# Kernel optimization log

Measured on AMD Instinct MI355X. Metric: run time of the kernel, lower is better.

The kernel has to match this reference:

```python
import jax, jax.numpy as jnp
import numpy as np

TAU = 2.0  # LIF membrane time constant (tau=2.0)
V_TH = 1.0  # spiking threshold (spikingjelly default)

@jax.custom_vjp
def spike(v):
    # Heaviside spike at v >= 0 (input is v - V_TH)
    return (v >= 0.0).astype(v.dtype)

def _spike_fwd(v):
    return spike(v), v

def _spike_bwd(v, g):
    # ATan surrogate gradient (spikingjelly default, alpha=2):
    # d/dv = alpha / (2 * (1 + (pi/2 * alpha * v)^2)) = 1 / (1 + (pi*v)^2)
    return (g / (1.0 + (jnp.pi * v) ** 2),)

spike.defvjp(_spike_fwd, _spike_bwd)

def lif_linear(x, w):
    """SpikLinearLayer: Linear (no bias) then multi-step LIF over leading T axis.
    x: [T, B, N, Din], w: [Dout, Din] -> spikes [T, B, N, Dout]
    LIF: v <- v + (y - v)/tau ; s = H(v - vth) ; hard reset v <- v*(1-s)
    """
    y = jnp.einsum('tbnd,ed->tbne', x, w)
    def step(v, yt):
        v = v + (yt - v) / TAU
        s = spike(v - V_TH)
        return v * (1.0 - s), s
    _, spikes = jax.lax.scan(step, jnp.zeros_like(y[0]), y)
    return spikes

def setup_inputs() -> dict:
    key = jax.random.key(0)
    k0, k1, k2, k3 = jax.random.split(key, 4)
    T, B, N, D, L = 4, 32, 1024, 256, 2
    x = jax.random.normal(k0, (T, B, N, D), dtype=jnp.float32)
    w_in = jax.random.normal(k1, (2 * D, D), dtype=jnp.float32) * 0.05
    w_hidden = jax.random.normal(k2, (L, 2 * D, 2 * D), dtype=jnp.float32) * 0.05
    w_out = jax.random.normal(k3, (D, 2 * D), dtype=jnp.float32) * 0.05
    return {"x": x, "w_in": w_in, "w_hidden": w_hidden, "w_out": w_out}

def reference(x, w_in, w_hidden, w_out):
    # TemporalBlock.forward
    h = lif_linear(x, w_in)                       # [T,B,N,2D]
    for l in range(w_hidden.shape[0]):
        h = h * (1.0 - lif_linear(h, w_hidden[l]))  # multiplicative spike gate
    return lif_linear(h, w_out)                   # [T,B,N,D]
```

## Files before the change

### kernel.cpp

```cpp
#include <hip/hip_runtime.h>
#include <stdint.h>

typedef __attribute__((ext_vector_type(8))) short short8;
typedef __attribute__((ext_vector_type(4))) float f32x4;

constexpr int T_ = 4;
constexpr int BNTOT = 32768;

__device__ __forceinline__ void gload_lds16(const void* g, void* lds) {
    __builtin_amdgcn_global_load_lds(
        (const __attribute__((address_space(1))) void*)g,
        (__attribute__((address_space(3))) void*)lds, 16, 0, 0);
}

__device__ __forceinline__ uint32_t bf1(float f) {
    uint32_t x = __builtin_bit_cast(uint32_t, f);
    return (x + 0x7FFFu + ((x >> 16) & 1u)) >> 16;
}
__device__ __forceinline__ uint32_t pk(float lo, float hi) {
    return bf1(lo) | (bf1(hi) << 16);
}

__global__ __launch_bounds__(256)
void cvt_bf16(const float* __restrict__ in, ushort* __restrict__ out) {
    const size_t i = ((size_t)blockIdx.x * 256 + threadIdx.x) * 8;
    const float4 a = *(const float4*)(in + i);
    const float4 b = *(const float4*)(in + i + 4);
    uint4 o;
    o.x = pk(a.x, a.y); o.y = pk(a.z, a.w);
    o.z = pk(b.x, b.y); o.w = pk(b.z, b.w);
    *(uint4*)(out + i) = o;
}

template <int MODE, int K, int NOUT>
__global__ __launch_bounds__(256, 2)
void lif_mfma(const ushort* __restrict__ A,
              const float* __restrict__ W,
              void* __restrict__ Out)
{
    __shared__ __align__(16) char smem[81920];

    constexpr int NS = K / 64;
    constexpr int NCOLT = NOUT / 64;

    const int tid = threadIdx.x;
    const int l   = tid & 63;
    const int w   = tid >> 6;

    const int id  = blockIdx.x;
    const int xcd = id & 7;
    const int j_  = id >> 3;
    const int row0 = (xcd * 64 + j_ / NCOLT) * 64;
    const int col0 = (j_ % NCOLT) * 64;

    const int rowbyte = (l & 15) << 7;
    const int gx = l >> 4;
    const int sw = l & 7;

    f32x4 acc[4][4];
#pragma unroll
    for (int m = 0; m < 4; ++m)
#pragma unroll
        for (int n = 0; n < 4; ++n) acc[m][n] = (f32x4)0.f;

    const int a_rowin = l >> 3;
    const int a_gsrc  = (l & 7) ^ a_rowin;
    const ushort* a_base = A + (size_t)(w * BNTOT + row0 + a_rowin) * K + a_gsrc * 8;

    const int bc  = tid >> 2;
    const int bkq = tid & 3;
    const float* w_base = W + (size_t)(col0 + bc) * K + bkq * 16;
    const int b_g0 = (bkq * 2)     ^ (bc & 7);
    const int b_g1 = (bkq * 2 + 1) ^ (bc & 7);

    auto stageA = [&](int s, int buf) {
        const ushort* ap = a_base + (size_t)s * 64;
        char* ad = smem + buf * 32768 + w * 8192;
#pragma unroll
        for (int i = 0; i < 8; ++i)
            gload_lds16(ap + (size_t)i * 8 * K, ad + i * 1024);
    };
    auto writeB = [&](const float4& b0, const float4& b1,
                      const float4& b2, const float4& b3, int buf) {
        char* bd = smem + 65536 + buf * 8192 + bc * 128;
        uint4 lo, hi;
        lo.x = pk(b0.x, b0.y); lo.y = pk(b0.z, b0.w);
        lo.z = pk(b1.x, b1.y); lo.w = pk(b1.z, b1.w);
        hi.x = pk(b2.x, b2.y); hi.y = pk(b2.z, b2.w);
        hi.z = pk(b3.x, b3.y); hi.w = pk(b3.z, b3.w);
        *(uint4*)(bd + b_g0 * 16) = lo;
        *(uint4*)(bd + b_g1 * 16) = hi;
    };

    {
        const float* wp = w_base;
        float4 b0 = *(const float4*)(wp);
        float4 b1 = *(const float4*)(wp + 4);
        float4 b2 = *(const float4*)(wp + 8);
        float4 b3 = *(const float4*)(wp + 12);
        stageA(0, 0);
        writeB(b0, b1, b2, b3, 0);
    }
    __syncthreads();

    int buf = 0;
    for (int s = 0; s < NS; ++s) {
        const bool more = (s + 1 < NS);
        float4 b0, b1, b2, b3;
        if (more) {
            const float* wp = w_base + (s + 1) * 64;
            b0 = *(const float4*)(wp);
            b1 = *(const float4*)(wp + 4);
            b2 = *(const float4*)(wp + 8);
            b3 = *(const float4*)(wp + 12);
            stageA(s + 1, buf ^ 1);
        }
        {
            const char* at = smem + buf * 32768 + w * 8192;
            const char* bt = smem + 65536 + buf * 8192;
#pragma unroll
            for (int kk = 0; kk < 2; ++kk) {
                const int go = (((kk * 4 + gx) ^ sw) << 4);
                short8 af[4], bfr[4];
#pragma unroll
                for (int m = 0; m < 4; ++m)
                    af[m] = *(const short8*)(at + m * 2048 + rowbyte + go);
#pragma unroll
                for (int n = 0; n < 4; ++n)
                    bfr[n] = *(const short8*)(bt + n * 2048 + rowbyte + go);
#pragma unroll
                for (int m = 0; m < 4; ++m)
#pragma unroll
                    for (int n = 0; n < 4; ++n)
                        acc[m][n] = __builtin_amdgcn_mfma_f32_16x16x32_bf16(
                            af[m], bfr[n], acc[m][n], 0, 0, 0);
            }
        }
        if (more) writeB(b0, b1, b2, b3, buf ^ 1);
        __syncthreads();
        buf ^= 1;
    }

    {
        float* Yw = (float*)smem + w * 4096;
#pragma unroll
        for (int m = 0; m < 4; ++m)
#pragma unroll
            for (int n = 0; n < 4; ++n)
#pragma unroll
                for (int j = 0; j < 4; ++j) {
                    const int row = m * 16 + gx * 4 + j;
                    const int colp = (n * 16 + (l & 15)) ^ (((row >> 2) & 1) << 4);
                    Yw[row * 64 + colp] = acc[m][n][j];
                }
    }
    __syncthreads();
    {
        const int rr0 = tid >> 5;
        const int c2  = (tid & 31) * 2;
#pragma unroll
        for (int rb = 0; rb < 8; ++rb) {
            const int row = rb * 8 + rr0;
            const int cp  = c2 ^ (((row >> 2) & 1) << 4);
            float v0 = 0.f, v1 = 0.f;
#pragma unroll
            for (int t = 0; t < T_; ++t) {
                const float* Yt = (const float*)smem + t * 4096 + row * 64;
                const float y0 = Yt[cp], y1 = Yt[cp + 1];
                v0 = 0.5f * (v0 + y0);
                v1 = 0.5f * (v1 + y1);
                const bool s0 = (v0 >= 1.f), s1 = (v1 >= 1.f);
                v0 = s0 ? 0.f : v0;
                v1 = s1 ? 0.f : v1;
                const size_t orow = (size_t)(t * BNTOT + row0 + row);
                if (MODE == 0) {
                    uint32_t u = (s0 ? 0x3F80u : 0u) | (s1 ? 0x3F800000u : 0u);
                    *(uint32_t*)((ushort*)Out + orow * NOUT + col0 + c2) = u;
                } else if (MODE == 1) {
                    const uint32_t h = *(const uint32_t*)(A + orow * K + col0 + c2);
                    const uint32_t msk = (s0 ? 0u : 0xFFFFu) | (s1 ? 0u : 0xFFFF0000u);
                    *(uint32_t*)((ushort*)Out + orow * NOUT + col0 + c2) = h & msk;
                } else {
                    float2 o;
                    o.x = s0 ? 1.f : 0.f;
                    o.y = s1 ? 1.f : 0.f;
                    *(float2*)((float*)Out + orow * NOUT + col0 + c2) = o;
                }
            }
        }
    }
}

extern "C" void kernel_launch(void* const* d_in, const int* in_sizes, int n_in,
                              void* d_out, int out_size, void* d_ws, size_t ws_size,
                              hipStream_t stream)
{
    const float* x     = (const float*)d_in[0];
    const float* w_in  = (const float*)d_in[1];
    const float* w_h   = (const float*)d_in[2];
    const float* w_out = (const float*)d_in[3];

    ushort* xbf = (ushort*)d_out;
    ushort* hA  = (ushort*)d_ws;
    ushort* hB  = (ushort*)d_out;
    float*  out = (float*)d_out;

    cvt_bf16<<<16384, 256, 0, stream>>>(x, xbf);

    lif_mfma<0, 256, 512><<<8 * 512, 256, 0, stream>>>(xbf, w_in, hA);
    lif_mfma<1, 512, 512><<<8 * 512, 256, 0, stream>>>(hA, w_h, hB);
    lif_mfma<1, 512, 512><<<8 * 512, 256, 0, stream>>>(hB, w_h + 512 * 512, hA);
    lif_mfma<2, 512, 256><<<4 * 512, 256, 0, stream>>>(hA, w_out, out);
}
```

Before: 421.2 us.

## Halve K-tile and LDS footprint to raise occupancy to four blocks per CU

The K step shrinks from 64 to 32, which halves the A/B LDS staging buffers, with new swizzles for the narrower rows. The epilogue now writes the accumulator tile in two 32-column halves so the 40KB buffer can hold it, and launch bounds rise to four blocks per CU. The aim is more resident waves to hide global-load latency. The cost is twice as many loop iterations and barriers, less MFMA work per sync, and extra barriers in the epilogue.

```diff
diff --git a/kernel.cpp b/kernel.cpp
--- a/kernel.cpp
+++ b/kernel.cpp
@@ -33,14 +33,14 @@
 }
 
 template <int MODE, int K, int NOUT>
-__global__ __launch_bounds__(256, 2)
+__global__ __launch_bounds__(256, 4)
 void lif_mfma(const ushort* __restrict__ A,
               const float* __restrict__ W,
               void* __restrict__ Out)
 {
-    __shared__ __align__(16) char smem[81920];
+    __shared__ __align__(16) char smem[40960];
 
-    constexpr int NS = K / 64;
+    constexpr int NS = K / 32;
     constexpr int NCOLT = NOUT / 64;
 
     const int tid = threadIdx.x;
@@ -53,9 +53,8 @@
     const int row0 = (xcd * 64 + j_ / NCOLT) * 64;
     const int col0 = (j_ % NCOLT) * 64;
 
-    const int rowbyte = (l & 15) << 7;
-    const int gx = l >> 4;
-    const int sw = l & 7;
+    const int rby = (l & 15) * 64;
+    const int gp  = ((l >> 4) ^ ((l >> 1) & 3)) << 4;
 
     f32x4 acc[4][4];
 #pragma unroll
@@ -63,131 +62,117 @@
 #pragma unroll
         for (int n = 0; n < 4; ++n) acc[m][n] = (f32x4)0.f;
 
-    const int a_rowin = l >> 3;
-    const int a_gsrc  = (l & 7) ^ a_rowin;
-    const ushort* a_base = A + (size_t)(w * BNTOT + row0 + a_rowin) * K + a_gsrc * 8;
+    const int a_gsrc = (l & 3) ^ ((l >> 3) & 3);
+    const ushort* a_base = A + ((size_t)(w * BNTOT + row0) + (l >> 2)) * K + a_gsrc * 8;
 
-    const int bc  = tid >> 2;
-    const int bkq = tid & 3;
-    const float* w_base = W + (size_t)(col0 + bc) * K + bkq * 16;
-    const int b_g0 = (bkq * 2)     ^ (bc & 7);
-    const int b_g1 = (bkq * 2 + 1) ^ (bc & 7);
+    const int b_col  = tid >> 2;
+    const int b_gsrc = (tid & 3) ^ ((tid >> 3) & 3);
+    const float* w_base = W + (size_t)(col0 + b_col) * K + b_gsrc * 8;
 
     auto stageA = [&](int s, int buf) {
-        const ushort* ap = a_base + (size_t)s * 64;
-        char* ad = smem + buf * 32768 + w * 8192;
+        const ushort* ap = a_base + s * 32;
+        char* ad = smem + buf * 16384 + w * 4096;
 #pragma unroll
-        for (int i = 0; i < 8; ++i)
-            gload_lds16(ap + (size_t)i * 8 * K, ad + i * 1024);
+        for (int j = 0; j < 4; ++j)
+            gload_lds16(ap + (size_t)j * 16 * K, ad + j * 1024);
     };
-    auto writeB = [&](const float4& b0, const float4& b1,
-                      const float4& b2, const float4& b3, int buf) {
-        char* bd = smem + 65536 + buf * 8192 + bc * 128;
-        uint4 lo, hi;
-        lo.x = pk(b0.x, b0.y); lo.y = pk(b0.z, b0.w);
-        lo.z = pk(b1.x, b1.y); lo.w = pk(b1.z, b1.w);
-        hi.x = pk(b2.x, b2.y); hi.y = pk(b2.z, b2.w);
-        hi.z = pk(b3.x, b3.y); hi.w = pk(b3.z, b3.w);
-        *(uint4*)(bd + b_g0 * 16) = lo;
-        *(uint4*)(bd + b_g1 * 16) = hi;
+    auto writeB = [&](const float4& f0, const float4& f1, int buf) {
+        uint4 o;
+        o.x = pk(f0.x, f0.y); o.y = pk(f0.z, f0.w);
+        o.z = pk(f1.x, f1.y); o.w = pk(f1.z, f1.w);
+        *(uint4*)(smem + 32768 + buf * 4096 + b_col * 64 + (tid & 3) * 16) = o;
     };
 
     {
-        const float* wp = w_base;
-        float4 b0 = *(const float4*)(wp);
-        float4 b1 = *(const float4*)(wp + 4);
-        float4 b2 = *(const float4*)(wp + 8);
-        float4 b3 = *(const float4*)(wp + 12);
+        const float4 f0 = *(const float4*)(w_base);
+        const float4 f1 = *(const float4*)(w_base + 4);
         stageA(0, 0);
-        writeB(b0, b1, b2, b3, 0);
+        writeB(f0, f1, 0);
     }
     __syncthreads();
 
     int buf = 0;
     for (int s = 0; s < NS; ++s) {
         const bool more = (s + 1 < NS);
-        float4 b0, b1, b2, b3;
+        float4 f0, f1;
         if (more) {
-            const float* wp = w_base + (s + 1) * 64;
-            b0 = *(const float4*)(wp);
-            b1 = *(const float4*)(wp + 4);
-            b2 = *(const float4*)(wp + 8);
-            b3 = *(const float4*)(wp + 12);
+            const float* wp = w_base + (s + 1) * 32;
+            f0 = *(const float4*)(wp);
+            f1 = *(const float4*)(wp + 4);
             stageA(s + 1, buf ^ 1);
         }
         {
-            const char* at = smem + buf * 32768 + w * 8192;
-            const char* bt = smem + 65536 + buf * 8192;
+            const char* at = smem + buf * 16384 + w * 4096;
+            const char* bt = smem + 32768 + buf * 4096;
+            short8 af[4], bfr[4];
 #pragma unroll
-            for (int kk = 0; kk < 2; ++kk) {
-                const int go = (((kk * 4 + gx) ^ sw) << 4);
-                short8 af[4], bfr[4];
+            for (int m = 0; m < 4; ++m)
+                af[m] = *(const short8*)(at + m * 1024 + rby + gp);
 #pragma unroll
-                for (int m = 0; m < 4; ++m)
-                    af[m] = *(const short8*)(at + m * 2048 + rowbyte + go);
+            for (int n = 0; n < 4; ++n)
+                bfr[n] = *(const short8*)(bt + n * 1024 + rby + gp);
+#pragma unroll
+            for (int m = 0; m < 4; ++m)
 #pragma unroll
                 for (int n = 0; n < 4; ++n)
-                    bfr[n] = *(const short8*)(bt + n * 2048 + rowbyte + go);
-#pragma unroll
-                for (int m = 0; m < 4; ++m)
-#pragma unroll
-                    for (int n = 0; n < 4; ++n)
-                        acc[m][n] = __builtin_amdgcn_mfma_f32_16x16x32_bf16(
-                            af[m], bfr[n], acc[m][n], 0, 0, 0);
-            }
+                    acc[m][n] = __builtin_amdgcn_mfma_f32_16x16x32_bf16(
+                        af[m], bfr[n], acc[m][n], 0, 0, 0);
         }
-        if (more) writeB(b0, b1, b2, b3, buf ^ 1);
+        if (more) writeB(f0, f1, buf ^ 1);
         __syncthreads();
         buf ^= 1;
     }
 
-    {
-        float* Yw = (float*)smem + w * 4096;
+    float* Y = (float*)smem;
 #pragma unroll
-        for (int m = 0; m < 4; ++m)
+    for (int half = 0; half < 2; ++half) {
 #pragma unroll
-            for (int n = 0; n < 4; ++n)
+        for (int nn = 0; nn < 2; ++nn) {
+            const int n = half * 2 + nn;
+#pragma unroll
+            for (int m = 0; m < 4; ++m)
 #pragma unroll
                 for (int j = 0; j < 4; ++j) {
-                    const int row = m * 16 + gx * 4 + j;
-                    const int colp = (n * 16 + (l & 15)) ^ (((row >> 2) & 1) << 4);
-                    Yw[row * 64 + colp] = acc[m][n][j];
+                    const int row = m * 16 + (l >> 4) * 4 + j;
+                    const int cl  = nn * 16 + (l & 15);
+                    const int colp = cl ^ (((row >> 2) & 1) << 4);
+                    Y[w * 2048 + row * 32 + colp] = acc[m][n][j];
                 }
-    }
-    __syncthreads();
-    {
-        const int rr0 = tid >> 5;
-        const int c2  = (tid & 31) * 2;
+        }
+        __syncthreads();
 #pragma unroll
-        for (int rb = 0; rb < 8; ++rb) {
-            const int row = rb * 8 + rr0;
-            const int cp  = c2 ^ (((row >> 2) & 1) << 4);
+        for (int u4 = 0; u4 < 4; ++u4) {
+            const int u   = u4 * 256 + tid;
+            const int row = u >> 4;
+            const int cp  = (u & 15) * 2;
+            const int colp = cp ^ (((row >> 2) & 1) << 4);
             float v0 = 0.f, v1 = 0.f;
 #pragma unroll
             for (int t = 0; t < T_; ++t) {
-                const float* Yt = (const float*)smem + t * 4096 + row * 64;
-                const float y0 = Yt[cp], y1 = Yt[cp + 1];
-                v0 = 0.5f * (v0 + y0);
-                v1 = 0.5f * (v1 + y1);
+                const float2 y = *(const float2*)&Y[t * 2048 + row * 32 + colp];
+                v0 = 0.5f * (v0 + y.x);
+                v1 = 0.5f * (v1 + y.y);
                 const bool s0 = (v0 >= 1.f), s1 = (v1 >= 1.f);
                 v0 = s0 ? 0.f : v0;
                 v1 = s1 ? 0.f : v1;
                 const size_t orow = (size_t)(t * BNTOT + row0 + row);
+                const int oc = col0 + half * 32 + cp;
                 if (MODE == 0) {
-                    uint32_t u = (s0 ? 0x3F80u : 0u) | (s1 ? 0x3F800000u : 0u);
-                    *(uint32_t*)((ushort*)Out + orow * NOUT + col0 + c2) = u;
+                    uint32_t uo = (s0 ? 0x3F80u : 0u) | (s1 ? 0x3F800000u : 0u);
+                    *(uint32_t*)((ushort*)Out + orow * NOUT + oc) = uo;
                 } else if (MODE == 1) {
-                    const uint32_t h = *(const uint32_t*)(A + orow * K + col0 + c2);
+                    const uint32_t h = *(const uint32_t*)(A + orow * K + oc);
                     const uint32_t msk = (s0 ? 0u : 0xFFFFu) | (s1 ? 0u : 0xFFFF0000u);
-                    *(uint32_t*)((ushort*)Out + orow * NOUT + col0 + c2) = h & msk;
+                    *(uint32_t*)((ushort*)Out + orow * NOUT + oc) = h & msk;
                 } else {
                     float2 o;
                     o.x = s0 ? 1.f : 0.f;
                     o.y = s1 ? 1.f : 0.f;
-                    *(float2*)((float*)Out + orow * NOUT + col0 + c2) = o;
+                    *(float2*)((float*)Out + orow * NOUT + oc) = o;
                 }
             }
         }
+        __syncthreads();
     }
 }
 
```

Result: slower. 441.6 us (+4.8%).
